# Optimization experiments

Hardware: AMD Instinct MI355X
Metric: run time of the kernel (lower is better)

The kernel has to match this reference:

```python
import jax, jax.numpy as jnp
from jax import lax
import numpy as np

D_MODEL = 1024
EXP = 2
D_INNER = EXP * D_MODEL
D_STATE = 16
D_CONV = 4
DT_RANK = 64  # ceil(d_model/16), mamba default
NUM_GROUPS = 4
BSZ, SEQ = 2, 2048
EPS = 1e-5


def setup_inputs() -> dict:
    key = jax.random.key(0)
    ks = jax.random.split(key, 10)
    def n(k, shape, s=0.02):
        return jax.random.normal(k, shape, jnp.float32) * s
    return dict(
        x=jax.random.normal(ks[0], (BSZ, SEQ, D_MODEL), jnp.float32),
        ln1_g=jnp.ones((D_MODEL,), jnp.float32), ln1_b=jnp.zeros((D_MODEL,), jnp.float32),
        ln2_g=jnp.ones((D_MODEL,), jnp.float32), ln2_b=jnp.zeros((D_MODEL,), jnp.float32),
        W1=n(ks[1], (EXP * D_MODEL, D_MODEL)), b1=jnp.zeros((EXP * D_MODEL,), jnp.float32),
        W2=n(ks[2], (D_MODEL, EXP * D_MODEL)), b2=jnp.zeros((D_MODEL,), jnp.float32),
        in_proj_w=n(ks[3], (2 * D_INNER, D_MODEL)),
        conv_w=n(ks[4], (D_INNER, 1, D_CONV), 0.2), conv_b=jnp.zeros((D_INNER,), jnp.float32),
        x_proj_w=n(ks[5], (DT_RANK + 2 * D_STATE, D_INNER)),
        dt_proj_w=n(ks[6], (D_INNER, DT_RANK), 0.1), dt_proj_b=n(ks[7], (D_INNER,), 0.5),
        A_log=jnp.tile(jnp.log(jnp.arange(1, D_STATE + 1, dtype=jnp.float32)), (D_INNER, 1)),
        D_param=jnp.ones((D_INNER,), jnp.float32),
        out_proj_w=n(ks[8], (D_MODEL, D_INNER)),
    )


def _layernorm(x, g, b):
    m = jnp.mean(x, -1, keepdims=True)
    v = jnp.var(x, -1, keepdims=True)
    return (x - m) * lax.rsqrt(v + EPS) * g + b


def _ste_sign(w):
    # sign quantization with straight-through estimator (groupwise split is a no-op for sign)
    return w + lax.stop_gradient(jnp.sign(w) - w)


def _quant_act_groupwise(x, b=8):
    # groups along seq dim (x.shape[1]); gamma is the abs-max over the whole group slab
    Qb = float(2 ** (b - 1))
    B_, L, D = x.shape
    g = x.reshape(B_, NUM_GROUPS, L // NUM_GROUPS, D)
    gamma = jnp.max(jnp.abs(g), axis=(0, 2, 3), keepdims=True)
    q = jnp.clip(g * Qb / (gamma + EPS), -Qb + EPS, Qb - EPS)
    return q.reshape(B_, L, D)


def _mamba(u, in_proj_w, conv_w, conv_b, x_proj_w, dt_proj_w, dt_proj_b, A_log, D_param, out_proj_w):
    B_, L, _ = u.shape
    xz = u @ in_proj_w.T                         # [B, L, 2*d_inner]
    xs, z = jnp.split(xz, 2, axis=-1)
    # depthwise causal conv1d
    xt = jnp.transpose(xs, (0, 2, 1))            # [B, d_inner, L]
    xt = lax.conv_general_dilated(xt, conv_w, (1,), [(D_CONV - 1, 0)],
                                  feature_group_count=D_INNER,
                                  dimension_numbers=('NCH', 'OIH', 'NCH'))
    xt = xt + conv_b[None, :, None]
    xs = jax.nn.silu(jnp.transpose(xt, (0, 2, 1)))  # [B, L, d_inner]
    x_dbl = xs @ x_proj_w.T                      # [B, L, dt_rank + 2*d_state]
    dt, Bm, Cm = jnp.split(x_dbl, [DT_RANK, DT_RANK + D_STATE], axis=-1)
    dt = jax.nn.softplus(dt @ dt_proj_w.T + dt_proj_b)   # [B, L, d_inner]
    A = -jnp.exp(A_log)                          # [d_inner, d_state]

    def step(h, inp):
        dt_s, B_s, C_s, x_s = inp                # [B,di], [B,ds], [B,ds], [B,di]
        dA = jnp.exp(dt_s[..., None] * A)        # [B, di, ds]
        h = h * dA + (dt_s * x_s)[..., None] * B_s[:, None, :]
        y = jnp.einsum('bds,bs->bd', h, C_s)
        return h, y

    tm = lambda a: jnp.transpose(a, (1, 0, 2))   # time-major
    h0 = jnp.zeros((B_, D_INNER, D_STATE), u.dtype)
    _, ys = lax.scan(step, h0, (tm(dt), tm(Bm), tm(Cm), tm(xs)))
    y = jnp.transpose(ys, (1, 0, 2)) + D_param * xs
    y = y * jax.nn.silu(z)
    return y @ out_proj_w.T


def reference(x, ln1_g, ln1_b, ln2_g, ln2_b, W1, b1, W2, b2,
              in_proj_w, conv_w, conv_b, x_proj_w, dt_proj_w, dt_proj_b,
              A_log, D_param, out_proj_w):
    qW1 = _ste_sign(W1)
    qW2 = _ste_sign(W2)
    gated = jnp.clip(_layernorm(x, ln1_g, ln1_b) @ qW1.T + b1, -1.0, 1.0)  # Hardtanh
    x = x + gated @ qW2.T + b2
    qx = _quant_act_groupwise(x)
    out = qx + _mamba(_layernorm(qx, ln2_g, ln2_b), in_proj_w, conv_w, conv_b,
                      x_proj_w, dt_proj_w, dt_proj_b, A_log, D_param, out_proj_w)
    return out
```

## Files before the change

kernel.cpp:

```cpp
#include <hip/hip_runtime.h>
#include <math.h>

#define D_MODEL 1024
#define D_INNER 2048
#define D_STATE 16
#define DT_RANK 64
#define BSZ 2
#define SEQ 2048
#define NTOK (BSZ*SEQ)
#define NCH  (BSZ*D_INNER)
#define NCHUNK 64
#define CLEN 32
#define EPS 1e-5f

typedef __attribute__((ext_vector_type(8))) short short8v;
typedef __attribute__((ext_vector_type(4))) float f32x4;

__device__ __forceinline__ float sgnf(float w) {
    return (w > 0.f) ? 1.f : ((w < 0.f) ? -1.f : 0.f);
}
__device__ __forceinline__ unsigned short f2bf(float f) {
    unsigned int x = __float_as_uint(f);
    x += 0x7fffu + ((x >> 16) & 1u);
    return (unsigned short)(x >> 16);
}
__device__ __forceinline__ float bf2f(unsigned short u) {
    return __uint_as_float(((unsigned int)u) << 16);
}
__device__ __forceinline__ void stage16(const unsigned short* g, unsigned short* l) {
    __builtin_amdgcn_global_load_lds(
        (const __attribute__((address_space(1))) unsigned int*)g,
        (__attribute__((address_space(3))) unsigned int*)l, 16, 0, 0);
}

#define F4_C1   524288
#define F4_C2   1048576
#define F4_C3   2097152
#define F4_C4   2146304
#define F4_C5   2179072
#define F4_C6   2703360
__global__ __launch_bounds__(256) void f2bf_all_kernel(
    const float* __restrict__ W1, const float* __restrict__ W2,
    const float* __restrict__ inpj, const float* __restrict__ xpj,
    const float* __restrict__ dtpj, const float* __restrict__ outpj,
    unsigned short* __restrict__ o_w1, unsigned short* __restrict__ o_w2,
    unsigned short* __restrict__ o_in, unsigned short* __restrict__ o_xp,
    unsigned short* __restrict__ o_dt, unsigned short* __restrict__ o_out,
    unsigned int* __restrict__ gma)
{
    int i = blockIdx.x * 256 + threadIdx.x;
    if (blockIdx.x == 0 && threadIdx.x < 4) gma[threadIdx.x] = 0u;
    if (i >= F4_C6) return;
    const float* src; unsigned short* dst; int off; bool sign = false;
    if (i < F4_C1)      { src = W1;   dst = o_w1;  off = i;          sign = true; }
    else if (i < F4_C2) { src = W2;   dst = o_w2;  off = i - F4_C1;  sign = true; }
    else if (i < F4_C3) { src = inpj; dst = o_in;  off = i - F4_C2; }
    else if (i < F4_C4) { src = xpj;  dst = o_xp;  off = i - F4_C3; }
    else if (i < F4_C5) { src = dtpj; dst = o_dt;  off = i - F4_C4; }
    else                { src = outpj;dst = o_out; off = i - F4_C5; }
    float4 v = reinterpret_cast<const float4*>(src)[off];
    if (sign) { v.x = sgnf(v.x); v.y = sgnf(v.y); v.z = sgnf(v.z); v.w = sgnf(v.w); }
    ushort4 o;
    o.x = f2bf(v.x); o.y = f2bf(v.y); o.z = f2bf(v.z); o.w = f2bf(v.w);
    reinterpret_cast<ushort4*>(dst)[off] = o;
}

__global__ __launch_bounds__(256) void ln_hilo_kernel(const float* __restrict__ x,
                                                      const float* __restrict__ g,
                                                      const float* __restrict__ b,
                                                      unsigned short* __restrict__ hi,
                                                      unsigned short* __restrict__ lo) {
    int row = blockIdx.x, tid = threadIdx.x;
    float4 v = reinterpret_cast<const float4*>(x + (size_t)row * D_MODEL)[tid];
    float s = v.x + v.y + v.z + v.w;
    float q = v.x*v.x + v.y*v.y + v.z*v.z + v.w*v.w;
    #pragma unroll
    for (int off = 32; off > 0; off >>= 1) { s += __shfl_down(s, off); q += __shfl_down(q, off); }
    __shared__ float rs[4], rq[4], smean, srstd;
    if ((tid & 63) == 0) { rs[tid >> 6] = s; rq[tid >> 6] = q; }
    __syncthreads();
    if (tid == 0) {
        float ts = rs[0]+rs[1]+rs[2]+rs[3], tq = rq[0]+rq[1]+rq[2]+rq[3];
        float mean = ts * (1.0f / D_MODEL);
        smean = mean;
        srstd = rsqrtf(tq * (1.0f / D_MODEL) - mean*mean + EPS);
    }
    __syncthreads();
    float mean = smean, rstd = srstd;
    float4 gg = reinterpret_cast<const float4*>(g)[tid];
    float4 bb = reinterpret_cast<const float4*>(b)[tid];
    float o[4];
    o[0] = (v.x-mean)*rstd*gg.x + bb.x; o[1] = (v.y-mean)*rstd*gg.y + bb.y;
    o[2] = (v.z-mean)*rstd*gg.z + bb.z; o[3] = (v.w-mean)*rstd*gg.w + bb.w;
    ushort4 h4, l4;
    h4.x = f2bf(o[0]); l4.x = f2bf(o[0] - bf2f(h4.x));
    h4.y = f2bf(o[1]); l4.y = f2bf(o[1] - bf2f(h4.y));
    h4.z = f2bf(o[2]); l4.z = f2bf(o[2] - bf2f(h4.z));
    h4.w = f2bf(o[3]); l4.w = f2bf(o[3] - bf2f(h4.w));
    reinterpret_cast<ushort4*>(hi + (size_t)row * D_MODEL)[tid] = h4;
    reinterpret_cast<ushort4*>(lo + (size_t)row * D_MODEL)[tid] = l4;
}

template<int EP, bool DUALA, int BN, bool KSPLIT>
__global__ __launch_bounds__(256) void mfma_gemm(
    const unsigned short* __restrict__ A, const unsigned short* __restrict__ A2,
    const unsigned short* __restrict__ B, float* __restrict__ C,
    unsigned short* __restrict__ Cb,
    int M, int N, int K, int sA, int sC,
    const float* __restrict__ bias, const float* __restrict__ addx, int sAdd,
    unsigned int* __restrict__ gma, int ksl)
{
    constexpr int NF = BN / 32;
    __shared__ __align__(16) unsigned short As[128*32];
    __shared__ __align__(16) unsigned short As2[DUALA ? 128*32 : 8];
    __shared__ __align__(16) unsigned short Bs[BN*32];
    __shared__ float redmax[4];
    const int tid = threadIdx.x;
    const int lane = tid & 63;
    const int w = tid >> 6;
    const int wm = w >> 1, wn = w & 1;
    const int row0 = blockIdx.y * 128, col0 = blockIdx.x * BN;
    const int srow = lane >> 2;
    const int scol = (lane & 3) * 8;

    int k_begin = 0, k_end = K;
    if (KSPLIT) {
        int z = blockIdx.z;
        k_begin = z * ksl; k_end = k_begin + ksl;
        C += (size_t)z * M * sC;
    }

    f32x4 acc[4][NF];
    #pragma unroll
    for (int m = 0; m < 4; ++m)
        #pragma unroll
        for (int n = 0; n < NF; ++n)
            acc[m][n] = (f32x4){0.f, 0.f, 0.f, 0.f};

    for (int k0 = k_begin; k0 < k_end; k0 += 32) {
        #pragma unroll
        for (int i = 0; i < 2; ++i) {
            const int rbase = w * 32 + i * 16;
            stage16(A + (size_t)(row0 + rbase + srow) * sA + k0 + scol, &As[rbase * 32]);
            if (DUALA)
                stage16(A2 + (size_t)(row0 + rbase + srow) * sA + k0 + scol, &As2[rbase * 32]);
        }
        #pragma unroll
        for (int i = 0; i < BN/64; ++i) {
            const int rbase = (BN == 128) ? (w * 32 + i * 16) : (w * 16);
            if (col0 + rbase < N)
                stage16(B + (size_t)(col0 + rbase + srow) * K + k0 + scol, &Bs[rbase * 32]);
        }
        __syncthreads();

        short8v af[4], bfr[NF], af2[4];
        const int fr = lane & 15, kg = (lane >> 4) * 8;
        #pragma unroll
        for (int m = 0; m < 4; ++m)
            af[m] = *reinterpret_cast<const short8v*>(&As[(wm*64 + m*16 + fr) * 32 + kg]);
        if (DUALA) {
            #pragma unroll
            for (int m = 0; m < 4; ++m)
                af2[m] = *reinterpret_cast<const short8v*>(&As2[(wm*64 + m*16 + fr) * 32 + kg]);
        }
        #pragma unroll
        for (int n = 0; n < NF; ++n)
            bfr[n] = *reinterpret_cast<const short8v*>(&Bs[(wn*(BN/2) + n*16 + fr) * 32 + kg]);

        #pragma unroll
        for (int m = 0; m < 4; ++m)
            #pragma unroll
            for (int n = 0; n < NF; ++n) {
                acc[m][n] = __builtin_amdgcn_mfma_f32_16x16x32_bf16(af[m], bfr[n], acc[m][n], 0, 0, 0);
                if (DUALA)
                    acc[m][n] = __builtin_amdgcn_mfma_f32_16x16x32_bf16(af2[m], bfr[n], acc[m][n], 0, 0, 0);
            }
        __syncthreads();
    }

    const int fc = lane & 15, r4 = (lane >> 4) * 4;
    float lmax = 0.0f;
    #pragma unroll
    for (int m = 0; m < 4; ++m) {
        const int grb = row0 + wm*64 + m*16 + r4;
        #pragma unroll
        for (int n = 0; n < NF; ++n) {
            const int gc = col0 + wn*(BN/2) + n*16 + fc;
            if (gc >= N) continue;
            #pragma unroll
            for (int j = 0; j < 4; ++j) {
                const int r = grb + j;
                float v = acc[m][n][j];
                if (EP == 0) {
                    C[(size_t)r*sC + gc] = v;
                } else if (EP == 1) {
                    v += bias[gc];
                    v = fminf(1.0f, fmaxf(-1.0f, v));
                    Cb[(size_t)r*sC + gc] = f2bf(v);
                } else if (EP == 3) {
                    float t = v + bias[gc];
                    C[(size_t)r*sC + gc] = fmaxf(t, 0.0f) + log1pf(__expf(-fabsf(t)));
                } else if (EP == 4) {
                    C[(size_t)r*sC + gc] = v + addx[(size_t)r*sAdd + gc];
                } else if (EP == 6) {
                    Cb[(size_t)r*sC + gc] = f2bf(v);
                } else {
                    v += bias[gc] + addx[(size_t)r*sAdd + gc];
                    C[(size_t)r*sC + gc] = v;
                    lmax = fmaxf(lmax, fabsf(v));
                }
            }
        }
    }
    if (EP == 7) {
        #pragma unroll
        for (int off = 32; off > 0; off >>= 1) lmax = fmaxf(lmax, __shfl_down(lmax, off));
        if (lane == 0) redmax[w] = lmax;
        __syncthreads();
        if (tid == 0) {
            float t = fmaxf(fmaxf(redmax[0], redmax[1]), fmaxf(redmax[2], redmax[3]));
            int g = (row0 & (SEQ - 1)) >> 9;
            atomicMax(gma + g, __float_as_uint(t));
        }
    }
}

__global__ __launch_bounds__(256) void xproj_combine_kernel(
    const float* __restrict__ part,
    float* __restrict__ xdbl,
    unsigned short* __restrict__ xdt)
{
    int i = blockIdx.x * 256 + threadIdx.x;
    if (i >= NTOK * 24) return;
    const size_t stride = (size_t)NTOK * 96 / 4;
    float4 v0 = reinterpret_cast<const float4*>(part)[i];
    float4 v1 = reinterpret_cast<const float4*>(part)[i + stride];
    float4 v2 = reinterpret_cast<const float4*>(part)[i + 2*stride];
    float4 v3 = reinterpret_cast<const float4*>(part)[i + 3*stride];
    float4 o;
    o.x = (v0.x + v1.x) + (v2.x + v3.x);
    o.y = (v0.y + v1.y) + (v2.y + v3.y);
    o.z = (v0.z + v1.z) + (v2.z + v3.z);
    o.w = (v0.w + v1.w) + (v2.w + v3.w);
    reinterpret_cast<float4*>(xdbl)[i] = o;
    int row = i / 24, c4 = i % 24;
    if (c4 < 16) {
        ushort4 u;
        u.x = f2bf(o.x); u.y = f2bf(o.y); u.z = f2bf(o.z); u.w = f2bf(o.w);
        reinterpret_cast<ushort4*>(xdt + (size_t)row * 64)[c4] = u;
    }
}

__global__ __launch_bounds__(256) void quant_ln_kernel(
    const float* __restrict__ x2, const unsigned int* __restrict__ gamma_bits,
    const float* __restrict__ g, const float* __restrict__ b,
    float* __restrict__ qx, unsigned short* __restrict__ u)
{
    int row = blockIdx.x, tid = threadIdx.x;
    int grp = (row & (SEQ - 1)) >> 9;
    float gamma = __uint_as_float(gamma_bits[grp]);
    float scale = 128.0f / (gamma + EPS);
    const float lo = -128.0f + EPS, hi = 128.0f - EPS;
    float4 v = reinterpret_cast<const float4*>(x2 + (size_t)row * D_MODEL)[tid];
    float4 qv;
    qv.x = fminf(hi, fmaxf(lo, v.x * scale));
    qv.y = fminf(hi, fmaxf(lo, v.y * scale));
    qv.z = fminf(hi, fmaxf(lo, v.z * scale));
    qv.w = fminf(hi, fmaxf(lo, v.w * scale));
    reinterpret_cast<float4*>(qx + (size_t)row * D_MODEL)[tid] = qv;
    float s = qv.x + qv.y + qv.z + qv.w;
    float q = qv.x*qv.x + qv.y*qv.y + qv.z*qv.z + qv.w*qv.w;
    #pragma unroll
    for (int off = 32; off > 0; off >>= 1) { s += __shfl_down(s, off); q += __shfl_down(q, off); }
    __shared__ float rs[4], rq[4], smean, srstd;
    if ((tid & 63) == 0) { rs[tid >> 6] = s; rq[tid >> 6] = q; }
    __syncthreads();
    if (tid == 0) {
        float ts = rs[0]+rs[1]+rs[2]+rs[3], tq = rq[0]+rq[1]+rq[2]+rq[3];
        float mean = ts * (1.0f / D_MODEL);
        smean = mean;
        srstd = rsqrtf(tq * (1.0f / D_MODEL) - mean*mean + EPS);
    }
    __syncthreads();
    float mean = smean, rstd = srstd;
    float4 gg = reinterpret_cast<const float4*>(g)[tid];
    float4 bb = reinterpret_cast<const float4*>(b)[tid];
    ushort4 o;
    o.x = f2bf((qv.x-mean)*rstd*gg.x + bb.x);
    o.y = f2bf((qv.y-mean)*rstd*gg.y + bb.y);
    o.z = f2bf((qv.z-mean)*rstd*gg.z + bb.z);
    o.w = f2bf((qv.w-mean)*rstd*gg.w + bb.w);
    reinterpret_cast<ushort4*>(u + (size_t)row * D_MODEL)[tid] = o;
}

__global__ __launch_bounds__(256) void conv_silu_kernel(const unsigned short* __restrict__ xz,
                                                        const float* __restrict__ conv_w,
                                                        const float* __restrict__ conv_b,
                                                        unsigned short* __restrict__ xcb) {
    int c = blockIdx.x * 256 + threadIdx.x;
    int m = blockIdx.y;
    int b = m >> 11, l = m & (SEQ - 1);
    float4 w4 = reinterpret_cast<const float4*>(conv_w)[c];
    float wv[4] = {w4.x, w4.y, w4.z, w4.w};
    float s = conv_b[c];
    const unsigned short* base = xz + ((size_t)b * SEQ) * 4096 + c;
    #pragma unroll
    for (int k = 0; k < 4; ++k) {
        int ll = l - 3 + k;
        if (ll >= 0) s += bf2f(base[(size_t)ll * 4096]) * wv[k];
    }
    float sig = 1.0f / (1.0f + __expf(-s));
    xcb[(size_t)m * D_INNER + c] = f2bf(s * sig);
}

__device__ __forceinline__ void make_dA(float dA[D_STATE], float dtv,
                                        const float* a, bool pw) {
    if (pw) {
        dA[0] = __expf(dtv * a[0]);
        #pragma unroll
        for (int s = 1; s < D_STATE; ++s) dA[s] = dA[s>>1] * dA[(s-1)>>1];
    } else {
        #pragma unroll
        for (int s = 0; s < D_STATE; ++s) dA[s] = __expf(dtv * a[s]);
    }
}

__global__ __launch_bounds__(256) void scan_partial_kernel(
    const float* __restrict__ dt, const unsigned short* __restrict__ xcb,
    const float* __restrict__ xdbl, const float* __restrict__ A_log,
    float* __restrict__ Lbuf, float* __restrict__ Sbuf)
{
    int gtid = blockIdx.x * 256 + threadIdx.x;
    int ch = gtid & (NCH - 1);
    int c  = gtid >> 12;
    int b = ch >> 11, d = ch & (D_INNER - 1);
    float a[D_STATE], h[D_STATE];
    bool pw = true;
    #pragma unroll
    for (int s = 0; s < D_STATE; ++s) {
        a[s] = -__expf(A_log[(size_t)d * D_STATE + s]);
        h[s] = 0.0f;
    }
    #pragma unroll
    for (int s = 1; s < D_STATE; ++s)
        pw = pw && (fabsf(a[s] - a[0]*(float)(s+1)) <= 1e-3f * fabsf(a[s]));

    size_t m0 = (size_t)b * SEQ + (size_t)c * CLEN;
    float Ssum = 0.0f;

    float dt_n = dt[m0 * D_INNER + d];
    float x_n  = bf2f(xcb[m0 * D_INNER + d]);
    float4 B_n[4];
    {
        const float* xd = xdbl + m0 * 96;
        #pragma unroll
        for (int i = 0; i < 4; ++i)
            B_n[i] = *reinterpret_cast<const float4*>(xd + DT_RANK + 4*i);
    }

    for (int l = 0; l < CLEN; ++l) {
        float dtv = dt_n, xv = x_n;
        float Bc[D_STATE];
        #pragma unroll
        for (int i = 0; i < 4; ++i) {
            Bc[4*i+0] = B_n[i].x; Bc[4*i+1] = B_n[i].y; Bc[4*i+2] = B_n[i].z; Bc[4*i+3] = B_n[i].w;
        }
        if (l + 1 < CLEN) {
            size_t m1 = m0 + l + 1;
            dt_n = dt[m1 * D_INNER + d];
            x_n  = bf2f(xcb[m1 * D_INNER + d]);
            const float* xd = xdbl + m1 * 96;
            #pragma unroll
            for (int i = 0; i < 4; ++i)
                B_n[i] = *reinterpret_cast<const float4*>(xd + DT_RANK + 4*i);
        }
        Ssum += dtv;
        float dx = dtv * xv;
        float dA[D_STATE];
        make_dA(dA, dtv, a, pw);
        #pragma unroll
        for (int s = 0; s < D_STATE; ++s)
            h[s] = h[s] * dA[s] + dx * Bc[s];
    }
    float4* Lp = reinterpret_cast<float4*>(Lbuf + (size_t)c * (NCH * D_STATE) + (size_t)ch * D_STATE);
    Lp[0] = make_float4(h[0], h[1], h[2], h[3]);
    Lp[1] = make_float4(h[4], h[5], h[6], h[7]);
    Lp[2] = make_float4(h[8], h[9], h[10], h[11]);
    Lp[3] = make_float4(h[12], h[13], h[14], h[15]);
    Sbuf[(size_t)c * NCH + ch] = Ssum;
}

__global__ __launch_bounds__(256) void scan_combine_kernel(
    float* __restrict__ LH, const float* __restrict__ Sbuf,
    const float* __restrict__ A_log)
{
    int gtid = blockIdx.x * 256 + threadIdx.x;
    int s = gtid & (D_STATE - 1);
    int ch = gtid >> 4;
    int d = ch & (D_INNER - 1);
    float a = -__expf(A_log[(size_t)d * D_STATE + s]);
    float h = 0.0f;
    #pragma unroll 4
    for (int c = 0; c < NCHUNK; ++c) {
        size_t idx = (size_t)c * (NCH * D_STATE) + (size_t)ch * D_STATE + s;
        float loc = LH[idx];
        LH[idx] = h;
        float P = __expf(a * Sbuf[(size_t)c * NCH + ch]);
        h = h * P + loc;
    }
}

__global__ __launch_bounds__(256) void scan_final_kernel(
    const float* __restrict__ dt, const unsigned short* __restrict__ xcb,
    const unsigned short* __restrict__ xzb, const float* __restrict__ xdbl,
    const float* __restrict__ A_log, const float* __restrict__ D_param,
    const float* __restrict__ Hin, unsigned short* __restrict__ yb)
{
    int gtid = blockIdx.x * 256 + threadIdx.x;
    int ch = gtid & (NCH - 1);
    int c  = gtid >> 12;
    int b = ch >> 11, d = ch & (D_INNER - 1);
    float a[D_STATE], h[D_STATE];
    {
        const float4* Hp = reinterpret_cast<const float4*>(
            Hin + (size_t)c * (NCH * D_STATE) + (size_t)ch * D_STATE);
        float4 h0 = Hp[0], h1 = Hp[1], h2 = Hp[2], h3 = Hp[3];
        h[0]=h0.x; h[1]=h0.y; h[2]=h0.z; h[3]=h0.w;
        h[4]=h1.x; h[5]=h1.y; h[6]=h1.z; h[7]=h1.w;
        h[8]=h2.x; h[9]=h2.y; h[10]=h2.z; h[11]=h2.w;
        h[12]=h3.x; h[13]=h3.y; h[14]=h3.z; h[15]=h3.w;
    }
    bool pw = true;
    #pragma unroll
    for (int s = 0; s < D_STATE; ++s)
        a[s] = -__expf(A_log[(size_t)d * D_STATE + s]);
    #pragma unroll
    for (int s = 1; s < D_STATE; ++s)
        pw = pw && (fabsf(a[s] - a[0]*(float)(s+1)) <= 1e-3f * fabsf(a[s]));
    float Dp = D_param[d];

    size_t m0 = (size_t)b * SEQ + (size_t)c * CLEN;
    float dt_n = dt[m0 * D_INNER + d];
    float x_n  = bf2f(xcb[m0 * D_INNER + d]);
    float z_n  = bf2f(xzb[m0 * 4096 + D_INNER + d]);
    float4 B_n[4], C_n[4];
    {
        const float* xd = xdbl + m0 * 96;
        #pragma unroll
        for (int i = 0; i < 4; ++i) {
            B_n[i] = *reinterpret_cast<const float4*>(xd + DT_RANK + 4*i);
            C_n[i] = *reinterpret_cast<const float4*>(xd + DT_RANK + D_STATE + 4*i);
        }
    }

    for (int l = 0; l < CLEN; ++l) {
        float dtv = dt_n, xv = x_n, zv = z_n;
        float Bc[D_STATE], Cc[D_STATE];
        #pragma unroll
        for (int i = 0; i < 4; ++i) {
            Bc[4*i+0] = B_n[i].x; Bc[4*i+1] = B_n[i].y; Bc[4*i+2] = B_n[i].z; Bc[4*i+3] = B_n[i].w;
            Cc[4*i+0] = C_n[i].x; Cc[4*i+1] = C_n[i].y; Cc[4*i+2] = C_n[i].z; Cc[4*i+3] = C_n[i].w;
        }
        if (l + 1 < CLEN) {
            size_t m1 = m0 + l + 1;
            dt_n = dt[m1 * D_INNER + d];
            x_n  = bf2f(xcb[m1 * D_INNER + d]);
            z_n  = bf2f(xzb[m1 * 4096 + D_INNER + d]);
            const float* xd = xdbl + m1 * 96;
            #pragma unroll
            for (int i = 0; i < 4; ++i) {
                B_n[i] = *reinterpret_cast<const float4*>(xd + DT_RANK + 4*i);
                C_n[i] = *reinterpret_cast<const float4*>(xd + DT_RANK + D_STATE + 4*i);
            }
        }
        float dx = dtv * xv;
        float yv = 0.0f;
        float dA[D_STATE];
        make_dA(dA, dtv, a, pw);
        #pragma unroll
        for (int s = 0; s < D_STATE; ++s) {
            h[s] = h[s] * dA[s] + dx * Bc[s];
            yv += h[s] * Cc[s];
        }
        yv += Dp * xv;
        float sig = 1.0f / (1.0f + __expf(-zv));
        yb[(m0 + l) * D_INNER + d] = f2bf(yv * (zv * sig));
    }
}

extern "C" void kernel_launch(void* const* d_in, const int* in_sizes, int n_in,
                              void* d_out, int out_size, void* d_ws, size_t ws_size,
                              hipStream_t stream) {
    const float* x         = (const float*)d_in[0];
    const float* ln1_g     = (const float*)d_in[1];
    const float* ln1_b     = (const float*)d_in[2];
    const float* ln2_g     = (const float*)d_in[3];
    const float* ln2_b     = (const float*)d_in[4];
    const float* W1        = (const float*)d_in[5];
    const float* b1        = (const float*)d_in[6];
    const float* W2        = (const float*)d_in[7];
    const float* b2        = (const float*)d_in[8];
    const float* in_proj   = (const float*)d_in[9];
    const float* conv_w    = (const float*)d_in[10];
    const float* conv_b    = (const float*)d_in[11];
    const float* x_proj    = (const float*)d_in[12];
    const float* dt_proj   = (const float*)d_in[13];
    const float* dt_proj_b = (const float*)d_in[14];
    const float* A_log     = (const float*)d_in[15];
    const float* D_param   = (const float*)d_in[16];
    const float* out_proj  = (const float*)d_in[17];
    float* out = (float*)d_out;

    char* ws = (char*)d_ws;
    float*          f_x2   = (float*)         (ws + 0);
    unsigned short* b_xz   = (unsigned short*)(ws + 16777216);
    float*          f_dt   = (float*)         (ws + 50331648);
    float*          f_xdbl = (float*)         (ws + 83886080);
    float*          f_L    = (float*)         (ws + 85458944);
    float*          f_xp   = f_L;
    float*          f_S    = (float*)         (ws + 102236160);
    unsigned int*   f_gamma= (unsigned int*)  (ws + 103284736);
    unsigned short* b_a1hi = (unsigned short*)(ws + 103284800);
    unsigned short* b_a1lo = b_a1hi + 4194304;
    unsigned short* b_y    = b_a1hi;
    unsigned short* b_gated= (unsigned short*)(ws + 120062016);
    unsigned short* b_xc   = b_gated;
    unsigned short* b_u    = (unsigned short*)(ws + 136839232);
    unsigned short* b_xdt  = b_u;
    unsigned short* b_w1s  = (unsigned short*)(ws + 145227840);
    unsigned short* b_w2s  = (unsigned short*)(ws + 149422144);
    unsigned short* b_inpj = (unsigned short*)(ws + 153616448);
    unsigned short* b_xpj  = (unsigned short*)(ws + 162005056);
    unsigned short* b_dtpj = (unsigned short*)(ws + 162398272);
    unsigned short* b_outpj= (unsigned short*)(ws + 162660416);

    dim3 b256(256);

    f2bf_all_kernel<<<dim3((F4_C6 + 255)/256), b256, 0, stream>>>(
        W1, W2, in_proj, x_proj, dt_proj, out_proj,
        b_w1s, b_w2s, b_inpj, b_xpj, b_dtpj, b_outpj, f_gamma);

    ln_hilo_kernel<<<dim3(NTOK), b256, 0, stream>>>(x, ln1_g, ln1_b, b_a1hi, b_a1lo);
    mfma_gemm<1, true, 64, false><<<dim3(32, 32), b256, 0, stream>>>(
        b_a1hi, b_a1lo, b_w1s, nullptr, b_gated, NTOK, D_INNER, D_MODEL, D_MODEL, D_INNER,
        b1, nullptr, 0, nullptr, 0);
    mfma_gemm<7, false, 64, false><<<dim3(16, 32), b256, 0, stream>>>(
        b_gated, nullptr, b_w2s, f_x2, nullptr, NTOK, D_MODEL, D_INNER, D_INNER, D_MODEL,
        b2, x, D_MODEL, f_gamma, 0);
    quant_ln_kernel<<<dim3(NTOK), b256, 0, stream>>>(f_x2, f_gamma, ln2_g, ln2_b, f_x2, b_u);
    mfma_gemm<6, false, 128, false><<<dim3(32, 32), b256, 0, stream>>>(
        b_u, nullptr, b_inpj, nullptr, b_xz, NTOK, 2*D_INNER, D_MODEL, D_MODEL, 2*D_INNER,
        nullptr, nullptr, 0, nullptr, 0);
    conv_silu_kernel<<<dim3(D_INNER/256, NTOK), b256, 0, stream>>>(b_xz, conv_w, conv_b, b_xc);
    mfma_gemm<0, false, 128, true><<<dim3(1, 32, 4), b256, 0, stream>>>(
        b_xc, nullptr, b_xpj, f_xp, nullptr, NTOK, DT_RANK + 2*D_STATE, D_INNER, D_INNER,
        DT_RANK + 2*D_STATE, nullptr, nullptr, 0, nullptr, 512);
    xproj_combine_kernel<<<dim3((NTOK*24 + 255)/256), b256, 0, stream>>>(f_xp, f_xdbl, b_xdt);
    mfma_gemm<3, false, 64, false><<<dim3(32, 32), b256, 0, stream>>>(
        b_xdt, nullptr, b_dtpj, f_dt, nullptr, NTOK, D_INNER, DT_RANK, DT_RANK, D_INNER,
        dt_proj_b, nullptr, 0, nullptr, 0);
    scan_partial_kernel<<<dim3(NCH*NCHUNK/256), b256, 0, stream>>>(
        f_dt, b_xc, f_xdbl, A_log, f_L, f_S);
    scan_combine_kernel<<<dim3(NCH*D_STATE/256), b256, 0, stream>>>(f_L, f_S, A_log);
    scan_final_kernel<<<dim3(NCH*NCHUNK/256), b256, 0, stream>>>(
        f_dt, b_xc, b_xz, f_xdbl, A_log, D_param, f_L, b_y);
    mfma_gemm<4, false, 64, false><<<dim3(16, 32), b256, 0, stream>>>(
        b_y, nullptr, b_outpj, out, nullptr, NTOK, D_MODEL, D_INNER, D_INNER, D_MODEL,
        nullptr, f_x2, D_MODEL, nullptr, 0);
}
```

Before: 478.2 us.

## Remap GEMM workgroups across XCDs, widen GEMM tiles, store dt in bf16

Remaps the linear workgroup index in non-split GEMMs so that consecutive blocks land on the same XCD, aiming for better L2 reuse. Widens the BN tile from 64 to 128 for the W1, W2 and out_proj GEMMs, halving their grid sizes. Stores softplus(dt) as bf16 instead of fp32, which halves dt traffic in both scan kernels but lowers dt precision. The larger tiles mean fewer blocks and possibly lower occupancy.

```diff
diff --git a/kernel.cpp b/kernel.cpp
--- a/kernel.cpp
+++ b/kernel.cpp
@@ -119,7 +119,16 @@
     const int lane = tid & 63;
     const int w = tid >> 6;
     const int wm = w >> 1, wn = w & 1;
-    const int row0 = blockIdx.y * 128, col0 = blockIdx.x * BN;
+
+    int bx = blockIdx.x, by = blockIdx.y;
+    if (!KSPLIT) {
+        const int gx = gridDim.x;
+        const int nwg = gx * gridDim.y;
+        int lin = by * gx + bx;
+        int nl = (lin & 7) * (nwg >> 3) + (lin >> 3);
+        bx = nl % gx; by = nl / gx;
+    }
+    const int row0 = by * 128, col0 = bx * BN;
     const int srow = lane >> 2;
     const int scol = (lane & 3) * 8;
 
@@ -199,7 +208,8 @@
                     Cb[(size_t)r*sC + gc] = f2bf(v);
                 } else if (EP == 3) {
                     float t = v + bias[gc];
-                    C[(size_t)r*sC + gc] = fmaxf(t, 0.0f) + log1pf(__expf(-fabsf(t)));
+                    t = fmaxf(t, 0.0f) + log1pf(__expf(-fabsf(t)));
+                    Cb[(size_t)r*sC + gc] = f2bf(t);
                 } else if (EP == 4) {
                     C[(size_t)r*sC + gc] = v + addx[(size_t)r*sAdd + gc];
                 } else if (EP == 6) {
@@ -326,7 +336,7 @@
 }
 
 __global__ __launch_bounds__(256) void scan_partial_kernel(
-    const float* __restrict__ dt, const unsigned short* __restrict__ xcb,
+    const unsigned short* __restrict__ dt, const unsigned short* __restrict__ xcb,
     const float* __restrict__ xdbl, const float* __restrict__ A_log,
     float* __restrict__ Lbuf, float* __restrict__ Sbuf)
 {
@@ -348,7 +358,7 @@
     size_t m0 = (size_t)b * SEQ + (size_t)c * CLEN;
     float Ssum = 0.0f;
 
-    float dt_n = dt[m0 * D_INNER + d];
+    float dt_n = bf2f(dt[m0 * D_INNER + d]);
     float x_n  = bf2f(xcb[m0 * D_INNER + d]);
     float4 B_n[4];
     {
@@ -367,7 +377,7 @@
         }
         if (l + 1 < CLEN) {
             size_t m1 = m0 + l + 1;
-            dt_n = dt[m1 * D_INNER + d];
+            dt_n = bf2f(dt[m1 * D_INNER + d]);
             x_n  = bf2f(xcb[m1 * D_INNER + d]);
             const float* xd = xdbl + m1 * 96;
             #pragma unroll
@@ -411,7 +421,7 @@
 }
 
 __global__ __launch_bounds__(256) void scan_final_kernel(
-    const float* __restrict__ dt, const unsigned short* __restrict__ xcb,
+    const unsigned short* __restrict__ dt, const unsigned short* __restrict__ xcb,
     const unsigned short* __restrict__ xzb, const float* __restrict__ xdbl,
     const float* __restrict__ A_log, const float* __restrict__ D_param,
     const float* __restrict__ Hin, unsigned short* __restrict__ yb)
@@ -440,7 +450,7 @@
     float Dp = D_param[d];
 
     size_t m0 = (size_t)b * SEQ + (size_t)c * CLEN;
-    float dt_n = dt[m0 * D_INNER + d];
+    float dt_n = bf2f(dt[m0 * D_INNER + d]);
     float x_n  = bf2f(xcb[m0 * D_INNER + d]);
     float z_n  = bf2f(xzb[m0 * 4096 + D_INNER + d]);
     float4 B_n[4], C_n[4];
@@ -463,7 +473,7 @@
         }
         if (l + 1 < CLEN) {
             size_t m1 = m0 + l + 1;
-            dt_n = dt[m1 * D_INNER + d];
+            dt_n = bf2f(dt[m1 * D_INNER + d]);
             x_n  = bf2f(xcb[m1 * D_INNER + d]);
             z_n  = bf2f(xzb[m1 * 4096 + D_INNER + d]);
             const float* xd = xdbl + m1 * 96;
@@ -514,7 +524,7 @@
     char* ws = (char*)d_ws;
     float*          f_x2   = (float*)         (ws + 0);
     unsigned short* b_xz   = (unsigned short*)(ws + 16777216);
-    float*          f_dt   = (float*)         (ws + 50331648);
+    unsigned short* b_dt   = (unsigned short*)(ws + 50331648);
     float*          f_xdbl = (float*)         (ws + 83886080);
     float*          f_L    = (float*)         (ws + 85458944);
     float*          f_xp   = f_L;
@@ -541,10 +551,10 @@
         b_w1s, b_w2s, b_inpj, b_xpj, b_dtpj, b_outpj, f_gamma);
 
     ln_hilo_kernel<<<dim3(NTOK), b256, 0, stream>>>(x, ln1_g, ln1_b, b_a1hi, b_a1lo);
-    mfma_gemm<1, true, 64, false><<<dim3(32, 32), b256, 0, stream>>>(
+    mfma_gemm<1, true, 128, false><<<dim3(16, 32), b256, 0, stream>>>(
         b_a1hi, b_a1lo, b_w1s, nullptr, b_gated, NTOK, D_INNER, D_MODEL, D_MODEL, D_INNER,
         b1, nullptr, 0, nullptr, 0);
-    mfma_gemm<7, false, 64, false><<<dim3(16, 32), b256, 0, stream>>>(
+    mfma_gemm<7, false, 128, false><<<dim3(8, 32), b256, 0, stream>>>(
         b_gated, nullptr, b_w2s, f_x2, nullptr, NTOK, D_MODEL, D_INNER, D_INNER, D_MODEL,
         b2, x, D_MODEL, f_gamma, 0);
     quant_ln_kernel<<<dim3(NTOK), b256, 0, stream>>>(f_x2, f_gamma, ln2_g, ln2_b, f_x2, b_u);
@@ -557,14 +567,14 @@
         DT_RANK + 2*D_STATE, nullptr, nullptr, 0, nullptr, 512);
     xproj_combine_kernel<<<dim3((NTOK*24 + 255)/256), b256, 0, stream>>>(f_xp, f_xdbl, b_xdt);
     mfma_gemm<3, false, 64, false><<<dim3(32, 32), b256, 0, stream>>>(
-        b_xdt, nullptr, b_dtpj, f_dt, nullptr, NTOK, D_INNER, DT_RANK, DT_RANK, D_INNER,
+        b_xdt, nullptr, b_dtpj, nullptr, b_dt, NTOK, D_INNER, DT_RANK, DT_RANK, D_INNER,
         dt_proj_b, nullptr, 0, nullptr, 0);
     scan_partial_kernel<<<dim3(NCH*NCHUNK/256), b256, 0, stream>>>(
-        f_dt, b_xc, f_xdbl, A_log, f_L, f_S);
+        b_dt, b_xc, f_xdbl, A_log, f_L, f_S);
     scan_combine_kernel<<<dim3(NCH*D_STATE/256), b256, 0, stream>>>(f_L, f_S, A_log);
     scan_final_kernel<<<dim3(NCH*NCHUNK/256), b256, 0, stream>>>(
-        f_dt, b_xc, b_xz, f_xdbl, A_log, D_param, f_L, b_y);
-    mfma_gemm<4, false, 64, false><<<dim3(16, 32), b256, 0, stream>>>(
+        b_dt, b_xc, b_xz, f_xdbl, A_log, D_param, f_L, b_y);
+    mfma_gemm<4, false, 128, false><<<dim3(8, 32), b256, 0, stream>>>(
         b_y, nullptr, b_outpj, out, nullptr, NTOK, D_MODEL, D_INNER, D_INNER, D_MODEL,
         nullptr, f_x2, D_MODEL, nullptr, 0);
 }
```

Result: no change. 473.1 us (-1.1%).
